# Performance work log

Hardware: AMD Instinct MI355X
Metric: run time of the kernel (lower is better)

The kernel has to match this reference:

```python
import jax, jax.numpy as jnp
import numpy as np

N_HEAD = 16
N_KV_HEAD = 4
HEAD_DIM = 128
D_MODEL = 2048
ROTARY_DIM = 128  # == head_dim
ROTARY_BASE = 10000
N_CTX = 2048
BATCH = 2
SEQ = 2048


def _rope_sincos(T, dtype):
    # Matches calculate_sin_cos_rotary with rotary_adjacent_pairs=False:
    # freq = base**(d/(rd/2)) for d in [0, rd/2), then tiled twice.
    pos = jnp.arange(T, dtype=jnp.float32)
    dim = jnp.arange(ROTARY_DIM // 2, dtype=jnp.float32)
    freq = jnp.asarray(ROTARY_BASE, jnp.float32) ** (dim / (ROTARY_DIM / 2))
    freq = jnp.concatenate([freq, freq])          # [rd]
    angles = pos[:, None] / freq[None, :]          # [T, rd]
    return jnp.sin(angles).astype(dtype), jnp.cos(angles).astype(dtype)


def _rotate_half(x):
    # rotate_every_two with adjacent_pairs=False: [-x2, x1] over halves
    n = x.shape[-1] // 2
    return jnp.concatenate([-x[..., n:], x[..., :n]], axis=-1)


def setup_inputs() -> dict:
    key = jax.random.key(0)
    kx, kq, kkv, kp = jax.random.split(key, 4)
    scale = 0.02
    return {
        "x": jax.random.normal(kx, (BATCH, SEQ, D_MODEL), jnp.float32),
        "Wq": jax.random.normal(kq, (D_MODEL, D_MODEL), jnp.float32) * scale,
        "Wkv": jax.random.normal(kkv, (2 * N_KV_HEAD * HEAD_DIM, D_MODEL), jnp.float32) * scale,
        "Wproj": jax.random.normal(kp, (D_MODEL, D_MODEL), jnp.float32) * scale,
    }


def reference(x, Wq, Wkv, Wproj):
    B, T, C = x.shape
    # QKV projections (torch Linear: y = x @ W.T)
    q = x @ Wq.T                                   # [B,T,C]
    kv = x @ Wkv.T                                 # [B,T,2*kv*hd]
    k, v = jnp.split(kv, 2, axis=2)
    q = q.reshape(B, T, N_HEAD, HEAD_DIM).transpose(0, 2, 1, 3)      # [B,H,T,d]
    k = k.reshape(B, T, N_KV_HEAD, HEAD_DIM).transpose(0, 2, 1, 3)   # [B,Hk,T,d]
    v = v.reshape(B, T, N_KV_HEAD, HEAD_DIM).transpose(0, 2, 1, 3)

    # RoPE: position_ids = arange(T) clamped at n_ctx-1 (identity for T<=n_ctx)
    sin, cos = _rope_sincos(T, q.dtype)            # [T, rd]
    sin = sin[None, None]                          # [1,1,T,rd]
    cos = cos[None, None]
    q = q * cos + _rotate_half(q) * sin
    k = k * cos + _rotate_half(k) * sin

    # GQA: expand kv heads (repeat_interleave along head dim)
    rep = N_HEAD // N_KV_HEAD
    k = jnp.repeat(k, rep, axis=1)                 # [B,H,T,d]
    v = jnp.repeat(v, rep, axis=1)

    # Causal SDPA
    scale = 1.0 / np.sqrt(HEAD_DIM)
    scores = jnp.einsum('bhqd,bhkd->bhqk', q, k) * scale
    causal = jnp.tril(jnp.ones((T, T), bool))
    scores = jnp.where(causal[None, None], scores, jnp.asarray(-jnp.inf, scores.dtype))
    attn = jax.nn.softmax(scores, axis=-1)
    y = jnp.einsum('bhqk,bhkd->bhqd', attn, v)     # [B,H,T,d]

    y = y.transpose(0, 2, 1, 3).reshape(B, T, C)
    return y @ Wproj.T
```

## Files before the change

### kernel.cpp

```cpp
#include <hip/hip_runtime.h>
#include <stdint.h>

#define T_SEQ 2048
#define D_MODEL 2048
#define N_KV 4
#define HD 128
#define QKV_W 3072

typedef unsigned short us;
typedef __attribute__((ext_vector_type(8))) short bf16x8;
typedef __attribute__((ext_vector_type(4))) float f32x4;
typedef __attribute__((ext_vector_type(8))) unsigned short u16x8;

__device__ __forceinline__ us f2bf(float f) {
  union { float f; unsigned int u; } v; v.f = f;
  unsigned int r = v.u + 0x7FFFu + ((v.u >> 16) & 1u);
  return (us)(r >> 16);
}
__device__ __forceinline__ float bf2f(us h) {
  union { unsigned int u; float f; } v; v.u = ((unsigned int)h) << 16;
  return v.f;
}

__device__ __forceinline__ void load_lds16(const void* g, void* l) {
  __builtin_amdgcn_global_load_lds(
      (const __attribute__((address_space(1))) void*)g,
      (__attribute__((address_space(3))) void*)l, 16, 0, 0);
}

__global__ void fill_diag(float* __restrict__ out, float val, int n) {
  int i = blockIdx.x * blockDim.x + threadIdx.x;
  if (i < n) out[i] = val;
}

__global__ void cast_f32_bf16(const float* __restrict__ src,
                              us* __restrict__ dst, int n8) {
  int i = blockIdx.x * blockDim.x + threadIdx.x;
  if (i >= n8) return;
  const float4* s = (const float4*)src + (size_t)i * 2;
  float4 a = s[0], b = s[1];
  u16x8 o;
  o[0] = f2bf(a.x); o[1] = f2bf(a.y); o[2] = f2bf(a.z); o[3] = f2bf(a.w);
  o[4] = f2bf(b.x); o[5] = f2bf(b.y); o[6] = f2bf(b.z); o[7] = f2bf(b.w);
  *((u16x8*)dst + i) = o;
}

template <typename OUT>
__global__ __launch_bounds__(256) void gemm_bt(
    const us* __restrict__ A, const us* __restrict__ B,
    OUT* __restrict__ C, int M, int N, int K) {
  __shared__ us As[2][128 * 32];
  __shared__ us Bs[2][128 * 32];

  const int tid  = threadIdx.x;
  const int lane = tid & 63;
  const int wave = tid >> 6;
  const int l15  = lane & 15;
  const int quad = lane >> 4;
  const int bm = blockIdx.x * 128;
  const int bn = blockIdx.y * 128;
  const int wm = (wave & 1) * 64;
  const int wn = (wave >> 1) * 64;

  f32x4 acc[4][4];
#pragma unroll
  for (int i = 0; i < 4; i++)
#pragma unroll
    for (int j = 0; j < 4; j++) acc[i][j] = (f32x4)0.f;

  const int srow = tid >> 2;
  const int scol = (tid & 3) * 8;
  const us* Ag = A + (size_t)(bm + srow) * K + scol;
  const us* Bg = B + (size_t)(bn + srow) * K + scol;
  const size_t rowskip = (size_t)64 * K;

#define STAGE(buf, koff)                                            \
  do {                                                              \
    load_lds16(Ag + (koff), &As[(buf)][tid * 8]);                   \
    load_lds16(Ag + (koff) + rowskip, &As[(buf)][tid * 8 + 2048]);  \
    load_lds16(Bg + (koff), &Bs[(buf)][tid * 8]);                   \
    load_lds16(Bg + (koff) + rowskip, &Bs[(buf)][tid * 8 + 2048]);  \
  } while (0)

  STAGE(0, 0);
  __syncthreads();

  int cur = 0;
  for (int k0 = 0; k0 < K; k0 += 32) {
    if (k0 + 32 < K) STAGE(cur ^ 1, k0 + 32);

    bf16x8 a[4], b[4];
#pragma unroll
    for (int mt = 0; mt < 4; mt++)
      a[mt] = *(const bf16x8*)&As[cur][(wm + mt * 16 + l15) * 32 + quad * 8];
#pragma unroll
    for (int nt = 0; nt < 4; nt++)
      b[nt] = *(const bf16x8*)&Bs[cur][(wn + nt * 16 + l15) * 32 + quad * 8];
#pragma unroll
    for (int mt = 0; mt < 4; mt++)
#pragma unroll
      for (int nt = 0; nt < 4; nt++)
        acc[mt][nt] = __builtin_amdgcn_mfma_f32_16x16x32_bf16(a[mt], b[nt], acc[mt][nt], 0, 0, 0);

    __syncthreads();
    cur ^= 1;
  }
#undef STAGE

#pragma unroll
  for (int mt = 0; mt < 4; mt++) {
    int row = bm + wm + mt * 16 + quad * 4;
#pragma unroll
    for (int nt = 0; nt < 4; nt++) {
      int col = bn + wn + nt * 16 + l15;
#pragma unroll
      for (int r = 0; r < 4; r++) {
        if constexpr (sizeof(OUT) == 4)
          C[(size_t)(row + r) * N + col] = acc[mt][nt][r];
        else
          C[(size_t)(row + r) * N + col] = f2bf(acc[mt][nt][r]);
      }
    }
  }
}

__global__ void rope_kernel(us* __restrict__ qkv) {
  const int row = blockIdx.x;
  const int t = row & (T_SEQ - 1);
  const int tid = threadIdx.x;
  const float L2_10K_64 = 13.287712379549449f / 64.f;
  us* rp = qkv + (size_t)row * QKV_W;

#pragma unroll
  for (int it = 0; it < 4; it++) {
    int idx = it * 256 + tid;
    int h = idx >> 6, i = idx & 63;
    int base = h * HD;
    float ang = (float)t * exp2f(-(float)i * L2_10K_64);
    float s, c; sincosf(ang, &s, &c);
    float x1 = bf2f(rp[base + i]);
    float x2 = bf2f(rp[base + i + 64]);
    rp[base + i]      = f2bf(x1 * c - x2 * s);
    rp[base + i + 64] = f2bf(x2 * c + x1 * s);
  }
  {
    int h = tid >> 6, i = tid & 63;
    int base = 2048 + h * HD;
    float ang = (float)t * exp2f(-(float)i * L2_10K_64);
    float s, c; sincosf(ang, &s, &c);
    float x1 = bf2f(rp[base + i]);
    float x2 = bf2f(rp[base + i + 64]);
    rp[base + i]      = f2bf(x1 * c - x2 * s);
    rp[base + i + 64] = f2bf(x2 * c + x1 * s);
  }
}

__device__ __forceinline__ int vperm(int d) { return ((d >> 3) ^ d) & 7; }

__global__ __launch_bounds__(256) void attn_kernel(
    const us* __restrict__ qkv, us* __restrict__ y) {
  __shared__ us Ks[64][136];
  __shared__ us Vt[128][64];
  __shared__ us Pl[4][2][16][40];

  const int tid  = threadIdx.x;
  const int lane = tid & 63;
  const int wave = tid >> 6;
  const int l15  = lane & 15;
  const int quad = lane >> 4;
  const int p  = blockIdx.x;
  const int bh = blockIdx.y;
  const int b  = bh >> 4;
  const int h  = bh & 15;
  const int hk = h >> 2;

  const us* base = qkv + (size_t)b * T_SEQ * QKV_W;
  const int kcol = 2048 + hk * HD;
  const int vcol = kcol + 512;
  const int skey = tid >> 4;
  const int skk  = (tid & 15) * 8;
  const float scale = 0.12751744f;

  for (int half = 0; half < 2; half++) {
    const int x  = half ? p : 31 - p;
    const int m0 = x * 64;

    bf16x8 qf[4];
    {
      const us* Qrow = base + (size_t)(m0 + wave * 16 + l15) * QKV_W + h * HD;
#pragma unroll
      for (int s = 0; s < 4; s++)
        qf[s] = *(const bf16x8*)&Qrow[s * 32 + quad * 8];
    }

    f32x4 O[8];
#pragma unroll
    for (int i = 0; i < 8; i++) O[i] = (f32x4)0.f;
    float mrun[4], lrun[4];
#pragma unroll
    for (int r = 0; r < 4; r++) { mrun[r] = -INFINITY; lrun[r] = 0.f; }

    uint4 kreg[4]; u16x8 vreg[4];
#pragma unroll
    for (int r = 0; r < 4; r++) {
      const us* row = base + (size_t)(skey + r * 16) * QKV_W;
      kreg[r] = *(const uint4*)(row + kcol + skk);
      vreg[r] = *(const u16x8*)(row + vcol + skk);
    }

    for (int j = 0; j <= x; j++) {
      __syncthreads();
#pragma unroll
      for (int r = 0; r < 4; r++) {
        int key = skey + r * 16;
        *(uint4*)&Ks[key][skk] = kreg[r];
#pragma unroll
        for (int i = 0; i < 8; i++) {
          int d = skk + i;
          Vt[d][key ^ (vperm(d) << 3)] = vreg[r][i];
        }
      }
      __syncthreads();

      if (j < x) {
        const int k0n = (j + 1) * 64;
#pragma unroll
        for (int r = 0; r < 4; r++) {
          const us* row = base + (size_t)(k0n + skey + r * 16) * QKV_W;
          kreg[r] = *(const uint4*)(row + kcol + skk);
          vreg[r] = *(const u16x8*)(row + vcol + skk);
        }
      }

      f32x4 S[4];
      __builtin_amdgcn_s_setprio(1);
#pragma unroll
      for (int nt = 0; nt < 4; nt++) {
        f32x4 sa = (f32x4)0.f;
#pragma unroll
        for (int ks = 0; ks < 4; ks++) {
          bf16x8 kf = *(const bf16x8*)&Ks[nt * 16 + l15][ks * 32 + quad * 8];
          sa = __builtin_amdgcn_mfma_f32_16x16x32_bf16(qf[ks], kf, sa, 0, 0, 0);
        }
        S[nt] = sa;
      }
      __builtin_amdgcn_s_setprio(0);

      const int row0 = m0 + wave * 16 + quad * 4;
      if (j == x) {
        const int k0 = j * 64;
#pragma unroll
        for (int nt = 0; nt < 4; nt++) {
          int col = k0 + nt * 16 + l15;
#pragma unroll
          for (int r = 0; r < 4; r++) {
            float v = S[nt][r] * scale;
            if (col > row0 + r) v = -INFINITY;
            S[nt][r] = v;
          }
        }
      } else {
#pragma unroll
        for (int nt = 0; nt < 4; nt++)
#pragma unroll
          for (int r = 0; r < 4; r++) S[nt][r] *= scale;
      }

      float pr[4][4];
#pragma unroll
      for (int r = 0; r < 4; r++) {
        float mx = fmaxf(fmaxf(S[0][r], S[1][r]), fmaxf(S[2][r], S[3][r]));
#pragma unroll
        for (int off = 1; off < 16; off <<= 1)
          mx = fmaxf(mx, __shfl_xor(mx, off, 64));
        float mnew = fmaxf(mrun[r], mx);
        float alpha = exp2f(mrun[r] - mnew);
        mrun[r] = mnew;
        float sum = 0.f;
#pragma unroll
        for (int nt = 0; nt < 4; nt++) {
          float pv = exp2f(S[nt][r] - mnew);
          pr[nt][r] = pv;
          sum += pv;
        }
        lrun[r] = lrun[r] * alpha + sum;
#pragma unroll
        for (int ot = 0; ot < 8; ot++) O[ot][r] *= alpha;
      }

#pragma unroll
      for (int kh = 0; kh < 2; kh++) {
#pragma unroll
        for (int nt = 0; nt < 2; nt++)
#pragma unroll
          for (int r = 0; r < 4; r++)
            Pl[wave][kh][quad * 4 + r][nt * 16 + l15] = f2bf(pr[kh * 2 + nt][r]);
        bf16x8 pf = *(const bf16x8*)&Pl[wave][kh][l15][quad * 8];
        __builtin_amdgcn_s_setprio(1);
#pragma unroll
        for (int ot = 0; ot < 8; ot++) {
          int dcol = ot * 16 + l15;
          bf16x8 vf = *(const bf16x8*)&Vt[dcol][(kh * 32 + quad * 8) ^ (vperm(dcol) << 3)];
          O[ot] = __builtin_amdgcn_mfma_f32_16x16x32_bf16(pf, vf, O[ot], 0, 0, 0);
        }
        __builtin_amdgcn_s_setprio(0);
      }
    }

    const int t_out = m0 + wave * 16 + quad * 4;
#pragma unroll
    for (int r = 0; r < 4; r++) {
      float s = lrun[r];
#pragma unroll
      for (int off = 1; off < 16; off <<= 1)
        s += __shfl_xor(s, off, 64);
      float inv_l = 1.f / s;
      us* yrow = y + (size_t)(b * T_SEQ + t_out + r) * D_MODEL + h * HD;
#pragma unroll
      for (int ot = 0; ot < 8; ot++)
        yrow[ot * 16 + l15] = f2bf(O[ot][r] * inv_l);
    }
  }
}

extern "C" void kernel_launch(void* const* d_in, const int* in_sizes, int n_in,
                              void* d_out, int out_size, void* d_ws, size_t ws_size,
                              hipStream_t stream) {
  const float* x     = (const float*)d_in[0];
  const float* Wq    = (const float*)d_in[1];
  const float* Wkv   = (const float*)d_in[2];
  const float* Wproj = (const float*)d_in[3];
  float* out = (float*)d_out;

  const size_t NX  = (size_t)4096 * 2048;
  const size_t NWQ = (size_t)2048 * 2048;
  const size_t NWK = (size_t)1024 * 2048;
  const size_t needed_ws = (NX + (NWQ + NWK) + NWQ + NX) * sizeof(us);

  int b0 = (n_in >= 1 && (size_t)in_sizes[0] == NX);
  int b1 = (n_in >= 2 && (size_t)in_sizes[1] == NWQ);
  int b2 = (n_in >= 3 && (size_t)in_sizes[2] == NWK);
  int b3 = (n_in >= 4 && (size_t)in_sizes[3] == NWQ);
  int ws_ok = (ws_size >= needed_ws);
  int out_ok = ((size_t)out_size == NX);
  if (!(n_in == 4 && b0 && b1 && b2 && b3 && ws_ok && out_ok)) {
    float code = 1.0e6f * (float)(n_in < 10 ? n_in : 9)
               + 1.0e5f * b0 + 1.0e4f * b1 + 1.0e3f * b2 + 1.0e2f * b3
               + 10.0f * ws_ok + 40.0f * out_ok;
    fill_diag<<<dim3((out_size + 255) / 256), dim3(256), 0, stream>>>(out, code, out_size);
    return;
  }

  us* xb     = (us*)d_ws;
  us* Wqkvb  = xb + NX;
  us* Wpb    = Wqkvb + NWQ + NWK;
  us* ybuf   = Wpb + NWQ;
  us* qkvbuf = (us*)d_out;

  dim3 blk(256);
  cast_f32_bf16<<<dim3((int)(NX  / 8 / 256)), blk, 0, stream>>>(x,     xb,          (int)(NX  / 8));
  cast_f32_bf16<<<dim3((int)(NWQ / 8 / 256)), blk, 0, stream>>>(Wq,    Wqkvb,       (int)(NWQ / 8));
  cast_f32_bf16<<<dim3((int)(NWK / 8 / 256)), blk, 0, stream>>>(Wkv,   Wqkvb + NWQ, (int)(NWK / 8));
  cast_f32_bf16<<<dim3((int)(NWQ / 8 / 256)), blk, 0, stream>>>(Wproj, Wpb,         (int)(NWQ / 8));

  gemm_bt<us><<<dim3(32, 24), blk, 0, stream>>>(xb, Wqkvb, qkvbuf, 4096, 3072, 2048);
  rope_kernel<<<dim3(4096), blk, 0, stream>>>(qkvbuf);
  attn_kernel<<<dim3(16, 32), blk, 0, stream>>>(qkvbuf, ybuf);
  gemm_bt<float><<<dim3(32, 16), blk, 0, stream>>>(ybuf, Wpb, out, 4096, 2048, 2048);
}
```

Before: 412.7 us.

## Replace GEMM with 256x256-tile 8-wave pipelined kernel using swizzled LDS

Both projection GEMMs now use a new 512-thread kernel that computes 256x256 output tiles with a K-step of 64. Global-to-LDS loads are split into quarter stages and interleaved with MFMA quarters under fine-grained barriers and vmcnt waits. The LDS layout is XOR-swizzled to avoid bank conflicts, and MFMA phases are wrapped in raised wave priority. This targets more data reuse per tile and better load/compute overlap. In exchange, tile counts drop to 192 and 128 blocks on a 256-CU part, which may underfill the device and raise register pressure.

```diff
diff --git a/kernel.cpp b/kernel.cpp
--- a/kernel.cpp
+++ b/kernel.cpp
@@ -45,74 +45,149 @@
   *((u16x8*)dst + i) = o;
 }
 
+#define GBAR()                                  \
+  do {                                          \
+    asm volatile("" ::: "memory");              \
+    __builtin_amdgcn_s_barrier();               \
+    asm volatile("" ::: "memory");              \
+  } while (0)
+#define VMCNT6() asm volatile("s_waitcnt vmcnt(6)" ::: "memory")
+#define VMCNT0() asm volatile("s_waitcnt vmcnt(0)" ::: "memory")
+
 template <typename OUT>
-__global__ __launch_bounds__(256) void gemm_bt(
+__global__ __launch_bounds__(512) void gemm_bt8(
     const us* __restrict__ A, const us* __restrict__ B,
     OUT* __restrict__ C, int M, int N, int K) {
-  __shared__ us As[2][128 * 32];
-  __shared__ us Bs[2][128 * 32];
+  __shared__ us As[2][16384];
+  __shared__ us Bs[2][16384];
 
   const int tid  = threadIdx.x;
   const int lane = tid & 63;
   const int wave = tid >> 6;
+  const int wm   = wave & 1;
+  const int wn   = wave >> 1;
   const int l15  = lane & 15;
   const int quad = lane >> 4;
-  const int bm = blockIdx.x * 128;
-  const int bn = blockIdx.y * 128;
-  const int wm = (wave & 1) * 64;
-  const int wn = (wave >> 1) * 64;
-
-  f32x4 acc[4][4];
-#pragma unroll
-  for (int i = 0; i < 4; i++)
+  const int bm = blockIdx.x * 256;
+  const int bn = blockIdx.y * 256;
+  const int wm8 = wm * 8;
+  const int wn4 = wn * 4;
+
+  const int ro = ((l15 << 5) | (quad << 3)) ^ ((l15 & 8) << 1);
+
+  const int s    = lane ^ ((lane & 32) >> 4);
+  const int srow = s >> 2;
+  const int schk = (s & 3) * 8;
+
+  const int R_Ae = (wave & 3) | ((wave & 4) << 1);
+  const int R_Al = R_Ae + 4;
+  const int R_Be = ((wave >> 1) << 2) | (wave & 1);
+  const int R_Bl = R_Be + 2;
+
+  const us* Ab = A + (size_t)bm * K;
+  const us* Bb = B + (size_t)bn * K;
+
+  f32x4 acc[8][4];
+#pragma unroll
+  for (int i = 0; i < 8; i++)
 #pragma unroll
     for (int j = 0; j < 4; j++) acc[i][j] = (f32x4)0.f;
 
-  const int srow = tid >> 2;
-  const int scol = (tid & 3) * 8;
-  const us* Ag = A + (size_t)(bm + srow) * K + scol;
-  const us* Bg = B + (size_t)(bn + srow) * K + scol;
-  const size_t rowskip = (size_t)64 * K;
-
-#define STAGE(buf, koff)                                            \
-  do {                                                              \
-    load_lds16(Ag + (koff), &As[(buf)][tid * 8]);                   \
-    load_lds16(Ag + (koff) + rowskip, &As[(buf)][tid * 8 + 2048]);  \
-    load_lds16(Bg + (koff), &Bs[(buf)][tid * 8]);                   \
-    load_lds16(Bg + (koff) + rowskip, &Bs[(buf)][tid * 8 + 2048]);  \
+  bf16x8 af[4][2], bf[4][2];
+
+#define STG(DST, PG, R, KT)                                                   \
+  do {                                                                        \
+    load_lds16((PG) + (size_t)((R) * 16 + srow) * K + (KT) * 64 + schk,       \
+               &(DST)[(((R) * 2 + 0) << 9) + (lane << 3)]);                   \
+    load_lds16((PG) + (size_t)((R) * 16 + srow) * K + (KT) * 64 + 32 + schk,  \
+               &(DST)[(((R) * 2 + 1) << 9) + (lane << 3)]);                   \
   } while (0)
 
-  STAGE(0, 0);
-  __syncthreads();
-
-  int cur = 0;
-  for (int k0 = 0; k0 < K; k0 += 32) {
-    if (k0 + 32 < K) STAGE(cur ^ 1, k0 + 32);
-
-    bf16x8 a[4], b[4];
-#pragma unroll
-    for (int mt = 0; mt < 4; mt++)
-      a[mt] = *(const bf16x8*)&As[cur][(wm + mt * 16 + l15) * 32 + quad * 8];
-#pragma unroll
-    for (int nt = 0; nt < 4; nt++)
-      b[nt] = *(const bf16x8*)&Bs[cur][(wn + nt * 16 + l15) * 32 + quad * 8];
-#pragma unroll
-    for (int mt = 0; mt < 4; mt++)
-#pragma unroll
-      for (int nt = 0; nt < 4; nt++)
-        acc[mt][nt] = __builtin_amdgcn_mfma_f32_16x16x32_bf16(a[mt], b[nt], acc[mt][nt], 0, 0, 0);
-
-    __syncthreads();
-    cur ^= 1;
-  }
-#undef STAGE
-
-#pragma unroll
-  for (int mt = 0; mt < 4; mt++) {
-    int row = bm + wm + mt * 16 + quad * 4;
+#define LDA4(BUF, MTB)                                                        \
+  _Pragma("unroll") for (int t = 0; t < 4; t++)                               \
+      _Pragma("unroll") for (int ks = 0; ks < 2; ks++)                        \
+          af[t][ks] = *(const bf16x8*)&As[BUF][(((wm8 + (MTB) + t) * 2 + ks)  \
+                                               << 9) + ro];
+
+#define LDB2(BUF, NTB)                                                        \
+  _Pragma("unroll") for (int t = 0; t < 2; t++)                               \
+      _Pragma("unroll") for (int ks = 0; ks < 2; ks++)                        \
+          bf[(NTB) + t][ks] = *(const bf16x8*)&Bs[BUF][                       \
+              (((wn4 + (NTB) + t) * 2 + ks) << 9) + ro];
+
+#define MQ(MH, NB)                                                            \
+  __builtin_amdgcn_s_setprio(1);                                              \
+  _Pragma("unroll") for (int t = 0; t < 4; t++)                               \
+      _Pragma("unroll") for (int u = 0; u < 2; u++)                           \
+          _Pragma("unroll") for (int ks = 0; ks < 2; ks++)                    \
+              acc[(MH) * 4 + t][(NB) + u] =                                   \
+                  __builtin_amdgcn_mfma_f32_16x16x32_bf16(                    \
+                      af[t][ks], bf[(NB) + u][ks],                            \
+                      acc[(MH) * 4 + t][(NB) + u], 0, 0, 0);                  \
+  __builtin_amdgcn_s_setprio(0);
+
+  STG(As[0], Ab, R_Ae, 0); STG(As[0], Ab, R_Al, 0);
+  STG(Bs[0], Bb, R_Be, 0); STG(Bs[0], Bb, R_Bl, 0);
+  STG(As[1], Ab, R_Ae, 1); STG(Bs[1], Bb, R_Be, 1); STG(Bs[1], Bb, R_Bl, 1);
+  VMCNT6();
+  GBAR();
+
+  const int NI = K >> 7;
+  for (int i = 0; i < NI - 1; i++) {
+    const int t0 = 2 * i;
+    LDA4(0, 0) LDB2(0, 0)
+    STG(As[1], Ab, R_Al, t0 + 1);
+    GBAR(); MQ(0, 0) GBAR();
+    LDB2(0, 2)
+    STG(As[0], Ab, R_Ae, t0 + 2);
+    GBAR(); MQ(0, 2) GBAR();
+    LDA4(0, 4)
+    STG(Bs[0], Bb, R_Be, t0 + 2);
+    GBAR(); MQ(1, 2) GBAR();
+    STG(Bs[0], Bb, R_Bl, t0 + 2);
+    GBAR(); MQ(1, 0) VMCNT6(); GBAR();
+    LDA4(1, 0) LDB2(1, 0)
+    STG(As[0], Ab, R_Al, t0 + 2);
+    GBAR(); MQ(0, 0) GBAR();
+    LDB2(1, 2)
+    STG(As[1], Ab, R_Ae, t0 + 3);
+    GBAR(); MQ(0, 2) GBAR();
+    LDA4(1, 4)
+    STG(Bs[1], Bb, R_Be, t0 + 3);
+    GBAR(); MQ(1, 2) GBAR();
+    STG(Bs[1], Bb, R_Bl, t0 + 3);
+    GBAR(); MQ(1, 0) VMCNT6(); GBAR();
+  }
+
+  {
+    const int t0 = 2 * NI - 2;
+    LDA4(0, 0) LDB2(0, 0)
+    STG(As[1], Ab, R_Al, t0 + 1);
+    GBAR(); MQ(0, 0) GBAR();
+    LDB2(0, 2)
+    GBAR(); MQ(0, 2) GBAR();
+    LDA4(0, 4)
+    GBAR(); MQ(1, 2) GBAR();
+    GBAR(); MQ(1, 0) VMCNT0(); GBAR();
+    LDA4(1, 0) LDB2(1, 0)
+    GBAR(); MQ(0, 0) GBAR();
+    LDB2(1, 2)
+    GBAR(); MQ(0, 2) GBAR();
+    LDA4(1, 4)
+    GBAR(); MQ(1, 2) GBAR();
+    MQ(1, 0)
+  }
+#undef STG
+#undef LDA4
+#undef LDB2
+#undef MQ
+
+#pragma unroll
+  for (int mt = 0; mt < 8; mt++) {
+    int row = bm + wm * 128 + mt * 16 + quad * 4;
 #pragma unroll
     for (int nt = 0; nt < 4; nt++) {
-      int col = bn + wn + nt * 16 + l15;
+      int col = bn + wn * 64 + nt * 16 + l15;
 #pragma unroll
       for (int r = 0; r < 4; r++) {
         if constexpr (sizeof(OUT) == 4)
@@ -363,8 +438,8 @@
   cast_f32_bf16<<<dim3((int)(NWK / 8 / 256)), blk, 0, stream>>>(Wkv,   Wqkvb + NWQ, (int)(NWK / 8));
   cast_f32_bf16<<<dim3((int)(NWQ / 8 / 256)), blk, 0, stream>>>(Wproj, Wpb,         (int)(NWQ / 8));
 
-  gemm_bt<us><<<dim3(32, 24), blk, 0, stream>>>(xb, Wqkvb, qkvbuf, 4096, 3072, 2048);
+  gemm_bt8<us><<<dim3(16, 12), dim3(512), 0, stream>>>(xb, Wqkvb, qkvbuf, 4096, 3072, 2048);
   rope_kernel<<<dim3(4096), blk, 0, stream>>>(qkvbuf);
   attn_kernel<<<dim3(16, 32), blk, 0, stream>>>(qkvbuf, ybuf);
-  gemm_bt<float><<<dim3(32, 16), blk, 0, stream>>>(ybuf, Wpb, out, 4096, 2048, 2048);
-}
+  gemm_bt8<float><<<dim3(16, 8), dim3(512), 0, stream>>>(ybuf, Wpb, out, 4096, 2048, 2048);
+}
```

Result: slower. 441.8 us (+7.0%).
